# Performance work log

Hardware: AMD Instinct MI355X
Metric: run time of the kernel (lower is better)

The kernel has to match this reference:

```python
import jax, jax.numpy as jnp
import numpy as np

NEG_BIG = -9e15

def setup_inputs() -> dict:
    key = jax.random.key(0)
    k1, k2, k3, k4 = jax.random.split(key, 4)
    N, Fin, Fout = 8192, 256, 128
    x = jax.random.normal(k1, (N, Fin), dtype=jnp.float32)
    adj = jax.random.randint(k2, (N, N), 0, 2, dtype=jnp.int32)
    # xavier-uniform-like init
    limW = float(np.sqrt(6.0 / (Fin + Fout)))
    W = jax.random.uniform(k3, (Fin, Fout), minval=-limW, maxval=limW, dtype=jnp.float32)
    lima = float(np.sqrt(6.0 / (2 * Fout + 1)))
    a = jax.random.uniform(k4, (2 * Fout, 1), minval=-lima, maxval=lima, dtype=jnp.float32)
    return {"x": x, "adj": adj, "W": W, "a": a}

def reference(x, adj, W, a, alpha=0.2):
    # h: (N, Fout)
    h = x @ W
    Fout = W.shape[1]
    # Split a into source/target halves: e[i,j] = leakyrelu(h_i·a1 + h_j·a2)
    a1, a2 = a[:Fout, 0], a[Fout:, 0]
    s = h @ a1  # (N,) row (source) scores
    t = h @ a2  # (N,) col (target) scores
    e = jax.nn.leaky_relu(s[:, None] + t[None, :], negative_slope=alpha)  # (N, N)
    e = jnp.where(adj > 0, e, NEG_BIG)
    attention = jax.nn.softmax(e, axis=1)
    # dropout omitted (eval mode / training=False)
    return attention @ h
```

## Files before the change

### kernel.cpp

```cpp
#include <hip/hip_runtime.h>
#include <hip/hip_bf16.h>

typedef __attribute__((ext_vector_type(8))) short short8;
typedef __attribute__((ext_vector_type(4))) short short4v;
typedef __attribute__((ext_vector_type(4))) float f32x4;

#define NR 8192
#define LOG2E 1.4426950408889634f

__device__ __forceinline__ short f2bf(float f) {
  return __builtin_bit_cast(short, __float2bfloat16(f));
}

__global__ __launch_bounds__(256) void k_gemm_h(const float* __restrict__ x,
                                                const float* __restrict__ W,
                                                const float* __restrict__ a,
                                                short* __restrict__ HT2,
                                                float* __restrict__ sv,
                                                float* __restrict__ tv) {
  __shared__ short WT[128][136];
  const int tid = threadIdx.x;
  const int w = tid >> 6;
  const int L = tid & 63;
  const int lm = L & 15;
  const int q = L >> 4;
  const int i0 = blockIdx.x * 64;

  f32x4 acc[8];
#pragma unroll
  for (int nn = 0; nn < 8; ++nn) acc[nn] = (f32x4){0.f, 0.f, 0.f, 0.f};

  for (int kc = 0; kc < 256; kc += 128) {
    if (kc) __syncthreads();
#pragma unroll
    for (int p = 0; p < 16; ++p) {
      int idx = p * 256 + tid;
      int k = idx >> 5;
      int f4 = (idx & 31) * 4;
      float4 v = *(const float4*)&W[(kc + k) * 128 + f4];
      WT[f4 + 0][k] = f2bf(v.x);
      WT[f4 + 1][k] = f2bf(v.y);
      WT[f4 + 2][k] = f2bf(v.z);
      WT[f4 + 3][k] = f2bf(v.w);
    }
    __syncthreads();
#pragma unroll
    for (int ks = 0; ks < 4; ++ks) {
      int row = i0 + 16 * w + lm;
      const float* xp = &x[(size_t)row * 256 + kc + ks * 32 + q * 8];
      float4 xa = *(const float4*)xp;
      float4 xb = *(const float4*)(xp + 4);
      short8 af;
      af[0] = f2bf(xa.x); af[1] = f2bf(xa.y); af[2] = f2bf(xa.z); af[3] = f2bf(xa.w);
      af[4] = f2bf(xb.x); af[5] = f2bf(xb.y); af[6] = f2bf(xb.z); af[7] = f2bf(xb.w);
#pragma unroll
      for (int nn = 0; nn < 8; ++nn) {
        short8 bf = *(const short8*)&WT[nn * 16 + lm][ks * 32 + q * 8];
        acc[nn] = __builtin_amdgcn_mfma_f32_16x16x32_bf16(af, bf, acc[nn], 0, 0, 0);
      }
    }
  }

  const int ib = i0 + 16 * w + 4 * q;
  const int tbase = (ib >> 5) * 4096 + (ib & 31);
  float a1v[8], a2v[8];
#pragma unroll
  for (int nn = 0; nn < 8; ++nn) {
    a1v[nn] = a[nn * 16 + lm];
    a2v[nn] = a[128 + nn * 16 + lm];
  }
  float sr[4] = {0.f, 0.f, 0.f, 0.f};
  float tr[4] = {0.f, 0.f, 0.f, 0.f};
#pragma unroll
  for (int nn = 0; nn < 8; ++nn) {
    int f = nn * 16 + lm;
    short4v o;
    o[0] = f2bf(acc[nn][0]);
    o[1] = f2bf(acc[nn][1]);
    o[2] = f2bf(acc[nn][2]);
    o[3] = f2bf(acc[nn][3]);
    *(short4v*)&HT2[tbase + f * 32] = o;
#pragma unroll
    for (int r = 0; r < 4; ++r) {
      sr[r] += acc[nn][r] * a1v[nn];
      tr[r] += acc[nn][r] * a2v[nn];
    }
  }
#pragma unroll
  for (int d = 1; d < 16; d <<= 1) {
#pragma unroll
    for (int r = 0; r < 4; ++r) {
      sr[r] += __shfl_xor(sr[r], d);
      tr[r] += __shfl_xor(tr[r], d);
    }
  }
  if (lm == 0) {
#pragma unroll
    for (int r = 0; r < 4; ++r) {
      sv[ib + r] = sr[r] * LOG2E;
      tv[ib + r] = tr[r] * LOG2E;
    }
  }
}

__global__ __launch_bounds__(64, 2) void k_flash(const int* __restrict__ adj,
                                                 const short* __restrict__ HT2,
                                                 const float* __restrict__ sv,
                                                 const float* __restrict__ tv,
                                                 float* __restrict__ part,
                                                 float* __restrict__ lpart) {
  __shared__ float eps[32 * 128];
  const int L = threadIdx.x;
  const int lm = L & 15;
  const int q = L >> 4;
  const int sp = blockIdx.x & 7;
  const int it = blockIdx.x >> 3;
  const int i0 = it * 32;

  const int row0 = i0 + lm;
  const int row1 = row0 + 16;
  const float s0 = sv[row0];
  const float s1 = sv[row1];
  const size_t ar0 = (size_t)row0 * NR;
  const size_t ar1 = (size_t)row1 * NR;

  f32x4 acc[2][8];
#pragma unroll
  for (int mm = 0; mm < 2; ++mm)
#pragma unroll
    for (int nn = 0; nn < 8; ++nn) acc[mm][nn] = (f32x4){0.f, 0.f, 0.f, 0.f};
  float l0 = 0.f, l1 = 0.f;

  const int tile0 = sp * 32;
  int jb = tile0 * 32 + q * 8;
  int4 sa00 = *(const int4*)&adj[ar0 + jb];
  int4 sa01 = *(const int4*)&adj[ar0 + jb + 4];
  int4 sa10 = *(const int4*)&adj[ar1 + jb];
  int4 sa11 = *(const int4*)&adj[ar1 + jb + 4];
  const short* tp = &HT2[tile0 * 4096 + (lm * 32 + q * 8)];
  short8 sbf[8];
#pragma unroll
  for (int nn = 0; nn < 8; ++nn) sbf[nn] = *(const short8*)&tp[nn * 512];
  float4 stv0 = *(const float4*)&tv[jb];
  float4 stv1 = *(const float4*)&tv[jb + 4];

#pragma unroll 4
  for (int t = 0; t < 32; ++t) {
    int4 a00 = sa00, a01 = sa01, a10 = sa10, a11 = sa11;
    short8 bf[8];
#pragma unroll
    for (int nn = 0; nn < 8; ++nn) bf[nn] = sbf[nn];
    float4 tv0 = stv0, tv1 = stv1;
    if (t + 1 < 32) {
      int jn = (tile0 + t + 1) * 32 + q * 8;
      sa00 = *(const int4*)&adj[ar0 + jn];
      sa01 = *(const int4*)&adj[ar0 + jn + 4];
      sa10 = *(const int4*)&adj[ar1 + jn];
      sa11 = *(const int4*)&adj[ar1 + jn + 4];
      const short* np = &HT2[(tile0 + t + 1) * 4096 + (lm * 32 + q * 8)];
#pragma unroll
      for (int nn = 0; nn < 8; ++nn) sbf[nn] = *(const short8*)&np[nn * 512];
      stv0 = *(const float4*)&tv[jn];
      stv1 = *(const float4*)&tv[jn + 4];
    }

    int av0[8] = {a00.x, a00.y, a00.z, a00.w, a01.x, a01.y, a01.z, a01.w};
    int av1[8] = {a10.x, a10.y, a10.z, a10.w, a11.x, a11.y, a11.z, a11.w};
    float tvl[8] = {tv0.x, tv0.y, tv0.z, tv0.w, tv1.x, tv1.y, tv1.z, tv1.w};
    short8 p0, p1;
#pragma unroll
    for (int e = 0; e < 8; ++e) {
      float v0 = s0 + tvl[e];
      float e0 = fmaxf(v0, 0.2f * v0);
      float pp0 = (av0[e] > 0) ? __builtin_amdgcn_exp2f(e0) : 0.f;
      l0 += pp0;
      p0[e] = f2bf(pp0);
      float v1 = s1 + tvl[e];
      float e1 = fmaxf(v1, 0.2f * v1);
      float pp1 = (av1[e] > 0) ? __builtin_amdgcn_exp2f(e1) : 0.f;
      l1 += pp1;
      p1[e] = f2bf(pp1);
    }
#pragma unroll
    for (int nn = 0; nn < 8; ++nn) {
      acc[0][nn] = __builtin_amdgcn_mfma_f32_16x16x32_bf16(p0, bf[nn], acc[0][nn], 0, 0, 0);
      acc[1][nn] = __builtin_amdgcn_mfma_f32_16x16x32_bf16(p1, bf[nn], acc[1][nn], 0, 0, 0);
    }
  }

#pragma unroll
  for (int mm = 0; mm < 2; ++mm)
#pragma unroll
    for (int nn = 0; nn < 8; ++nn)
#pragma unroll
      for (int r = 0; r < 4; ++r)
        eps[(16 * mm + 4 * q + r) * 128 + nn * 16 + lm] = acc[mm][nn][r];
  float* pbase = part + ((size_t)sp * NR + i0) * 128;
#pragma unroll
  for (int c = 0; c < 16; ++c) {
    int idx = (c * 64 + L) * 4;
    *(float4*)&pbase[idx] = *(const float4*)&eps[idx];
  }

  l0 += __shfl_xor(l0, 16);
  l0 += __shfl_xor(l0, 32);
  l1 += __shfl_xor(l1, 16);
  l1 += __shfl_xor(l1, 32);
  if (q == 0) {
    lpart[sp * NR + row0] = l0;
    lpart[sp * NR + row1] = l1;
  }
}

__global__ __launch_bounds__(256) void k_reduce(const float* __restrict__ part,
                                                const float* __restrict__ lpart,
                                                float* __restrict__ out, int S) {
  int idx4 = blockIdx.x * 256 + threadIdx.x;
  int idx = idx4 * 4;
  int i = idx >> 7;
  float4 sum = {0.f, 0.f, 0.f, 0.f};
  for (int sp = 0; sp < S; ++sp) {
    float4 v = *(const float4*)&part[(size_t)sp * (NR * 128) + idx];
    sum.x += v.x; sum.y += v.y; sum.z += v.z; sum.w += v.w;
  }
  float l = 0.f;
  for (int sp = 0; sp < S; ++sp) l += lpart[sp * NR + i];
  float inv = (l > 0.f) ? 1.f / l : 0.f;
  float4 o = {sum.x * inv, sum.y * inv, sum.z * inv, sum.w * inv};
  *(float4*)&out[idx] = o;
}

extern "C" void kernel_launch(void* const* d_in, const int* in_sizes, int n_in,
                              void* d_out, int out_size, void* d_ws, size_t ws_size,
                              hipStream_t stream) {
  const float* x = (const float*)d_in[0];
  const int* adj = (const int*)d_in[1];
  const float* W = (const float*)d_in[2];
  const float* a = (const float*)d_in[3];
  float* out = (float*)d_out;

  char* ws = (char*)d_ws;
  short* HT2 = (short*)(ws + 0);
  float* sv = (float*)(ws + 2097152);
  float* tv = (float*)(ws + 2129920);
  float* lpart = (float*)(ws + 2162688);
  float* part = (float*)(ws + 2424832);

  const int S = 8;

  hipLaunchKernelGGL(k_gemm_h, dim3(128), dim3(256), 0, stream, x, W, a, HT2, sv, tv);
  hipLaunchKernelGGL(k_flash, dim3(256 * S), dim3(64), 0, stream, adj, HT2, sv, tv,
                     part, lpart);
  hipLaunchKernelGGL(k_reduce, dim3((NR * 128) / 1024), dim3(256), 0, stream, part,
                     lpart, out, S);
}
```

Measured before the change: 450.7 us.

## Factor exp of leaky-relu scores into precomputed row/column exponentials, raise split-K

Replaces the per-element exp2 of leaky_relu(s+t) with a product of precomputed exponentials: exp2(s)*exp2(t) when the positive branch applies, otherwise exp2(0.2s)*exp2(0.2t), with the branch chosen by comparing the product to 1. Column exponentials are produced in the GEMM kernel, and row exponentials are computed once per block. It also doubles the column split to 16, removes the register double-buffer of H tiles in favour of direct loads, halves the shared-memory epilogue buffer and raises the occupancy hint. The partial buffer grows, so the reduce kernel reads twice as much, and the unbounded exponentials risk overflow or precision loss for large scores.

```diff
diff --git a/kernel.cpp b/kernel.cpp
--- a/kernel.cpp
+++ b/kernel.cpp
@@ -17,7 +17,8 @@
                                                 const float* __restrict__ a,
                                                 short* __restrict__ HT2,
                                                 float* __restrict__ sv,
-                                                float* __restrict__ tv) {
+                                                float* __restrict__ etv,
+                                                float* __restrict__ etv2) {
   __shared__ short WT[128][136];
   const int tid = threadIdx.x;
   const int w = tid >> 6;
@@ -98,29 +99,34 @@
 #pragma unroll
     for (int r = 0; r < 4; ++r) {
       sv[ib + r] = sr[r] * LOG2E;
-      tv[ib + r] = tr[r] * LOG2E;
-    }
-  }
-}
-
-__global__ __launch_bounds__(64, 2) void k_flash(const int* __restrict__ adj,
+      float tl = tr[r] * LOG2E;
+      etv[ib + r] = __builtin_amdgcn_exp2f(tl);
+      etv2[ib + r] = __builtin_amdgcn_exp2f(0.2f * tl);
+    }
+  }
+}
+
+__global__ __launch_bounds__(64, 3) void k_flash(const int* __restrict__ adj,
                                                  const short* __restrict__ HT2,
                                                  const float* __restrict__ sv,
-                                                 const float* __restrict__ tv,
+                                                 const float* __restrict__ etv,
+                                                 const float* __restrict__ etv2,
                                                  float* __restrict__ part,
                                                  float* __restrict__ lpart) {
-  __shared__ float eps[32 * 128];
+  __shared__ float eps[16 * 128];
   const int L = threadIdx.x;
   const int lm = L & 15;
   const int q = L >> 4;
-  const int sp = blockIdx.x & 7;
-  const int it = blockIdx.x >> 3;
+  const int sp = blockIdx.x & 15;
+  const int it = blockIdx.x >> 4;
   const int i0 = it * 32;
 
   const int row0 = i0 + lm;
   const int row1 = row0 + 16;
-  const float s0 = sv[row0];
-  const float s1 = sv[row1];
+  const float Es0 = __builtin_amdgcn_exp2f(sv[row0]);
+  const float Es0b = __builtin_amdgcn_exp2f(0.2f * sv[row0]);
+  const float Es1 = __builtin_amdgcn_exp2f(sv[row1]);
+  const float Es1b = __builtin_amdgcn_exp2f(0.2f * sv[row1]);
   const size_t ar0 = (size_t)row0 * NR;
   const size_t ar1 = (size_t)row1 * NR;
 
@@ -131,53 +137,49 @@
     for (int nn = 0; nn < 8; ++nn) acc[mm][nn] = (f32x4){0.f, 0.f, 0.f, 0.f};
   float l0 = 0.f, l1 = 0.f;
 
-  const int tile0 = sp * 32;
+  const int tile0 = sp * 16;
   int jb = tile0 * 32 + q * 8;
   int4 sa00 = *(const int4*)&adj[ar0 + jb];
   int4 sa01 = *(const int4*)&adj[ar0 + jb + 4];
   int4 sa10 = *(const int4*)&adj[ar1 + jb];
   int4 sa11 = *(const int4*)&adj[ar1 + jb + 4];
-  const short* tp = &HT2[tile0 * 4096 + (lm * 32 + q * 8)];
-  short8 sbf[8];
-#pragma unroll
-  for (int nn = 0; nn < 8; ++nn) sbf[nn] = *(const short8*)&tp[nn * 512];
-  float4 stv0 = *(const float4*)&tv[jb];
-  float4 stv1 = *(const float4*)&tv[jb + 4];
 
 #pragma unroll 4
-  for (int t = 0; t < 32; ++t) {
+  for (int t = 0; t < 16; ++t) {
     int4 a00 = sa00, a01 = sa01, a10 = sa10, a11 = sa11;
-    short8 bf[8];
-#pragma unroll
-    for (int nn = 0; nn < 8; ++nn) bf[nn] = sbf[nn];
-    float4 tv0 = stv0, tv1 = stv1;
-    if (t + 1 < 32) {
+    if (t + 1 < 16) {
       int jn = (tile0 + t + 1) * 32 + q * 8;
       sa00 = *(const int4*)&adj[ar0 + jn];
       sa01 = *(const int4*)&adj[ar0 + jn + 4];
       sa10 = *(const int4*)&adj[ar1 + jn];
       sa11 = *(const int4*)&adj[ar1 + jn + 4];
-      const short* np = &HT2[(tile0 + t + 1) * 4096 + (lm * 32 + q * 8)];
-#pragma unroll
-      for (int nn = 0; nn < 8; ++nn) sbf[nn] = *(const short8*)&np[nn * 512];
-      stv0 = *(const float4*)&tv[jn];
-      stv1 = *(const float4*)&tv[jn + 4];
-    }
+    }
+    const int tile = tile0 + t;
+    const int jc = tile * 32 + q * 8;
+    float4 et0 = *(const float4*)&etv[jc];
+    float4 et1 = *(const float4*)&etv[jc + 4];
+    float4 eu0 = *(const float4*)&etv2[jc];
+    float4 eu1 = *(const float4*)&etv2[jc + 4];
+    const short* tp = &HT2[tile * 4096 + (lm * 32 + q * 8)];
+    short8 bf[8];
+#pragma unroll
+    for (int nn = 0; nn < 8; ++nn) bf[nn] = *(const short8*)&tp[nn * 512];
 
     int av0[8] = {a00.x, a00.y, a00.z, a00.w, a01.x, a01.y, a01.z, a01.w};
     int av1[8] = {a10.x, a10.y, a10.z, a10.w, a11.x, a11.y, a11.z, a11.w};
-    float tvl[8] = {tv0.x, tv0.y, tv0.z, tv0.w, tv1.x, tv1.y, tv1.z, tv1.w};
+    float etl[8] = {et0.x, et0.y, et0.z, et0.w, et1.x, et1.y, et1.z, et1.w};
+    float eul[8] = {eu0.x, eu0.y, eu0.z, eu0.w, eu1.x, eu1.y, eu1.z, eu1.w};
     short8 p0, p1;
 #pragma unroll
     for (int e = 0; e < 8; ++e) {
-      float v0 = s0 + tvl[e];
-      float e0 = fmaxf(v0, 0.2f * v0);
-      float pp0 = (av0[e] > 0) ? __builtin_amdgcn_exp2f(e0) : 0.f;
+      float pe0 = Es0 * etl[e];
+      float pn0 = Es0b * eul[e];
+      float pp0 = (av0[e] > 0) ? ((pe0 > 1.f) ? pe0 : pn0) : 0.f;
       l0 += pp0;
       p0[e] = f2bf(pp0);
-      float v1 = s1 + tvl[e];
-      float e1 = fmaxf(v1, 0.2f * v1);
-      float pp1 = (av1[e] > 0) ? __builtin_amdgcn_exp2f(e1) : 0.f;
+      float pe1 = Es1 * etl[e];
+      float pn1 = Es1b * eul[e];
+      float pp1 = (av1[e] > 0) ? ((pe1 > 1.f) ? pe1 : pn1) : 0.f;
       l1 += pp1;
       p1[e] = f2bf(pp1);
     }
@@ -189,17 +191,18 @@
   }
 
 #pragma unroll
-  for (int mm = 0; mm < 2; ++mm)
+  for (int mm = 0; mm < 2; ++mm) {
 #pragma unroll
     for (int nn = 0; nn < 8; ++nn)
 #pragma unroll
       for (int r = 0; r < 4; ++r)
-        eps[(16 * mm + 4 * q + r) * 128 + nn * 16 + lm] = acc[mm][nn][r];
-  float* pbase = part + ((size_t)sp * NR + i0) * 128;
-#pragma unroll
-  for (int c = 0; c < 16; ++c) {
-    int idx = (c * 64 + L) * 4;
-    *(float4*)&pbase[idx] = *(const float4*)&eps[idx];
+        eps[(4 * q + r) * 128 + nn * 16 + lm] = acc[mm][nn][r];
+    float* pbase = part + ((size_t)sp * NR + i0 + 16 * mm) * 128;
+#pragma unroll
+    for (int c = 0; c < 8; ++c) {
+      int idx = (c * 64 + L) * 4;
+      *(float4*)&pbase[idx] = *(const float4*)&eps[idx];
+    }
   }
 
   l0 += __shfl_xor(l0, 16);
@@ -242,15 +245,17 @@
   char* ws = (char*)d_ws;
   short* HT2 = (short*)(ws + 0);
   float* sv = (float*)(ws + 2097152);
-  float* tv = (float*)(ws + 2129920);
-  float* lpart = (float*)(ws + 2162688);
-  float* part = (float*)(ws + 2424832);
-
-  const int S = 8;
-
-  hipLaunchKernelGGL(k_gemm_h, dim3(128), dim3(256), 0, stream, x, W, a, HT2, sv, tv);
-  hipLaunchKernelGGL(k_flash, dim3(256 * S), dim3(64), 0, stream, adj, HT2, sv, tv,
-                     part, lpart);
+  float* etv = (float*)(ws + 2129920);
+  float* etv2 = (float*)(ws + 2162688);
+  float* lpart = (float*)(ws + 2195456);
+  float* part = (float*)(ws + 2719744);
+
+  const int S = 16;
+
+  hipLaunchKernelGGL(k_gemm_h, dim3(128), dim3(256), 0, stream, x, W, a, HT2, sv,
+                     etv, etv2);
+  hipLaunchKernelGGL(k_flash, dim3(256 * S), dim3(64), 0, stream, adj, HT2, sv,
+                     etv, etv2, part, lpart);
   hipLaunchKernelGGL(k_reduce, dim3((NR * 128) / 1024), dim3(256), 0, stream, part,
                      lpart, out, S);
 }
```

Result: slower. 513.5 us (+13.9%).

## Share HT2 tiles across four waves through swizzled LDS in flash kernel

Applied to the files above, without the earlier changes.

The attention kernel now runs 256-thread blocks covering 128 rows instead of 64-thread blocks covering 32 rows. Each block stages eight HT2 column tiles at a time into an XOR-swizzled 64 KB LDS buffer, so the four waves share one copy instead of each reading it from global memory. The column split grows from 8 to 16, which shortens each block's loop but doubles the partial sums the reduce kernel has to read. Register prefetching of HT2 and tv is removed, and barriers are added around each LDS refill, so load latency is less hidden.

```diff
diff --git a/kernel.cpp b/kernel.cpp
--- a/kernel.cpp
+++ b/kernel.cpp
@@ -103,21 +103,24 @@
   }
 }
 
-__global__ __launch_bounds__(64, 2) void k_flash(const int* __restrict__ adj,
-                                                 const short* __restrict__ HT2,
-                                                 const float* __restrict__ sv,
-                                                 const float* __restrict__ tv,
-                                                 float* __restrict__ part,
-                                                 float* __restrict__ lpart) {
-  __shared__ float eps[32 * 128];
-  const int L = threadIdx.x;
+__global__ __launch_bounds__(256, 2) void k_flash(const int* __restrict__ adj,
+                                                  const short* __restrict__ HT2,
+                                                  const float* __restrict__ sv,
+                                                  const float* __restrict__ tv,
+                                                  float* __restrict__ part,
+                                                  float* __restrict__ lpart) {
+  __shared__ short lds_s[32768];
+  unsigned* ldsw = (unsigned*)lds_s;
+  const int tid = threadIdx.x;
+  const int w = tid >> 6;
+  const int L = tid & 63;
   const int lm = L & 15;
   const int q = L >> 4;
-  const int sp = blockIdx.x & 7;
-  const int it = blockIdx.x >> 3;
-  const int i0 = it * 32;
-
-  const int row0 = i0 + lm;
+  const int sp = blockIdx.x & 15;
+  const int it = blockIdx.x >> 4;
+  const int i0 = it * 128;
+
+  const int row0 = i0 + 32 * w + lm;
   const int row1 = row0 + 16;
   const float s0 = sv[row0];
   const float s1 = sv[row1];
@@ -131,37 +134,46 @@
     for (int nn = 0; nn < 8; ++nn) acc[mm][nn] = (f32x4){0.f, 0.f, 0.f, 0.f};
   float l0 = 0.f, l1 = 0.f;
 
-  const int tile0 = sp * 32;
+  const int tile0 = sp * 16;
   int jb = tile0 * 32 + q * 8;
   int4 sa00 = *(const int4*)&adj[ar0 + jb];
   int4 sa01 = *(const int4*)&adj[ar0 + jb + 4];
   int4 sa10 = *(const int4*)&adj[ar1 + jb];
   int4 sa11 = *(const int4*)&adj[ar1 + jb + 4];
-  const short* tp = &HT2[tile0 * 4096 + (lm * 32 + q * 8)];
-  short8 sbf[8];
-#pragma unroll
-  for (int nn = 0; nn < 8; ++nn) sbf[nn] = *(const short8*)&tp[nn * 512];
-  float4 stv0 = *(const float4*)&tv[jb];
-  float4 stv1 = *(const float4*)&tv[jb + 4];
-
-#pragma unroll 4
-  for (int t = 0; t < 32; ++t) {
+
+  for (int t = 0; t < 16; ++t) {
+    if ((t & 7) == 0) {
+      __syncthreads();
+      const int pbase_t = tile0 + t;
+#pragma unroll
+      for (int z = 0; z < 16; ++z) {
+        int id = z * 256 + tid;
+        int tt = id >> 9;
+        int k = id & 511;
+        int f = k >> 2, c = k & 3;
+        uint4 v = *(const uint4*)&HT2[(size_t)(pbase_t + tt) * 4096 + k * 8];
+        int cs = c ^ ((f >> 1) & 3);
+        *(uint4*)&ldsw[tt * 2048 + f * 16 + cs * 4] = v;
+      }
+      __syncthreads();
+    }
     int4 a00 = sa00, a01 = sa01, a10 = sa10, a11 = sa11;
-    short8 bf[8];
-#pragma unroll
-    for (int nn = 0; nn < 8; ++nn) bf[nn] = sbf[nn];
-    float4 tv0 = stv0, tv1 = stv1;
-    if (t + 1 < 32) {
+    if (t + 1 < 16) {
       int jn = (tile0 + t + 1) * 32 + q * 8;
       sa00 = *(const int4*)&adj[ar0 + jn];
       sa01 = *(const int4*)&adj[ar0 + jn + 4];
       sa10 = *(const int4*)&adj[ar1 + jn];
       sa11 = *(const int4*)&adj[ar1 + jn + 4];
-      const short* np = &HT2[(tile0 + t + 1) * 4096 + (lm * 32 + q * 8)];
-#pragma unroll
-      for (int nn = 0; nn < 8; ++nn) sbf[nn] = *(const short8*)&np[nn * 512];
-      stv0 = *(const float4*)&tv[jn];
-      stv1 = *(const float4*)&tv[jn + 4];
+    }
+    const int jc = (tile0 + t) * 32 + q * 8;
+    float4 tv0 = *(const float4*)&tv[jc];
+    float4 tv1 = *(const float4*)&tv[jc + 4];
+    const int tt = t & 7;
+    short8 bf[8];
+#pragma unroll
+    for (int nn = 0; nn < 8; ++nn) {
+      int f = nn * 16 + lm;
+      bf[nn] = *(const short8*)&ldsw[tt * 2048 + f * 16 + ((q ^ ((f >> 1) & 3)) * 4)];
     }
 
     int av0[8] = {a00.x, a00.y, a00.z, a00.w, a01.x, a01.y, a01.z, a01.w};
@@ -187,19 +199,22 @@
       acc[1][nn] = __builtin_amdgcn_mfma_f32_16x16x32_bf16(p1, bf[nn], acc[1][nn], 0, 0, 0);
     }
   }
-
-#pragma unroll
-  for (int mm = 0; mm < 2; ++mm)
+  __syncthreads();
+
+  float* my = (float*)lds_s + w * 2048;
+#pragma unroll
+  for (int mm = 0; mm < 2; ++mm) {
 #pragma unroll
     for (int nn = 0; nn < 8; ++nn)
 #pragma unroll
       for (int r = 0; r < 4; ++r)
-        eps[(16 * mm + 4 * q + r) * 128 + nn * 16 + lm] = acc[mm][nn][r];
-  float* pbase = part + ((size_t)sp * NR + i0) * 128;
-#pragma unroll
-  for (int c = 0; c < 16; ++c) {
-    int idx = (c * 64 + L) * 4;
-    *(float4*)&pbase[idx] = *(const float4*)&eps[idx];
+        my[(4 * q + r) * 128 + nn * 16 + lm] = acc[mm][nn][r];
+    float* pbase = part + ((size_t)sp * NR + i0 + 32 * w + 16 * mm) * 128;
+#pragma unroll
+    for (int c = 0; c < 8; ++c) {
+      int idx = (c * 64 + L) * 4;
+      *(float4*)&pbase[idx] = *(const float4*)&my[idx];
+    }
   }
 
   l0 += __shfl_xor(l0, 16);
@@ -244,12 +259,12 @@
   float* sv = (float*)(ws + 2097152);
   float* tv = (float*)(ws + 2129920);
   float* lpart = (float*)(ws + 2162688);
-  float* part = (float*)(ws + 2424832);
-
-  const int S = 8;
+  float* part = (float*)(ws + 2719744);
+
+  const int S = 16;
 
   hipLaunchKernelGGL(k_gemm_h, dim3(128), dim3(256), 0, stream, x, W, a, HT2, sv, tv);
-  hipLaunchKernelGGL(k_flash, dim3(256 * S), dim3(64), 0, stream, adj, HT2, sv, tv,
+  hipLaunchKernelGGL(k_flash, dim3(64 * S), dim3(256), 0, stream, adj, HT2, sv, tv,
                      part, lpart);
   hipLaunchKernelGGL(k_reduce, dim3((NR * 128) / 1024), dim3(256), 0, stream, part,
                      lpart, out, S);
```

Result: faster. 423.6 us (-6.0%).
